# Performance work log

Hardware: AMD Instinct MI355X
Metric: run time of the kernel (lower is better)

The kernel has to match this reference:

```python
import jax, jax.numpy as jnp
import numpy as np

B, N, C = 8, 8192, 256
H = 8            # num_heads
D = C // H       # head dim = 32
P = 64           # proj_size (Linformer rank)


def setup_inputs() -> dict:
    key = jax.random.key(0)
    ks = jax.random.split(key, 12)
    s = lambda fan_in: 1.0 / np.sqrt(fan_in)
    return {
        "x": jax.random.normal(ks[0], (B, N, C), jnp.float32),
        "Wqkvv": jax.random.normal(ks[1], (4 * C, C), jnp.float32) * s(C),
        "WE": jax.random.normal(ks[2], (P, N), jnp.float32) * s(N),
        "bE": jax.random.normal(ks[3], (P,), jnp.float32) * s(N),
        "WF": jax.random.normal(ks[4], (P, N), jnp.float32) * s(N),
        "bF": jax.random.normal(ks[5], (P,), jnp.float32) * s(N),
        "Wo1": jax.random.normal(ks[6], (C // 2, C), jnp.float32) * s(C),
        "bo1": jax.random.normal(ks[7], (C // 2,), jnp.float32) * s(C),
        "Wo2": jax.random.normal(ks[8], (C // 2, C), jnp.float32) * s(C),
        "bo2": jax.random.normal(ks[9], (C // 2,), jnp.float32) * s(C),
        "temp1": jnp.ones((H, 1, 1), jnp.float32),
        "temp2": jnp.ones((H, 1, 1), jnp.float32),
    }


def _l2norm(v, axis=-1, eps=1e-12):
    # matches torch F.normalize
    n = jnp.sqrt(jnp.sum(v * v, axis=axis, keepdims=True))
    return v / jnp.maximum(n, eps)


def reference(x, Wqkvv, WE, bE, WF, bF, Wo1, bo1, Wo2, bo2, temp1, temp2):
    b, n, c = x.shape
    # qkvv: [b,n,4c] -> [4,b,h,d,n]  (includes the .transpose(-2,-1) of each part)
    qkvv = jnp.einsum('bnc,fc->bnf', x, Wqkvv).reshape(b, n, 4, H, D)
    qkvv = qkvv.transpose(2, 0, 3, 4, 1)
    q, k, v_ca, v_sa = qkvv[0], qkvv[1], qkvv[2], qkvv[3]  # each [b,h,d,n]

    # Linformer-style low-rank projections along the token axis
    k_proj = jnp.einsum('bhdn,pn->bhdp', k, WE) + bE   # [b,h,d,p]
    v_proj = jnp.einsum('bhdn,pn->bhdp', v_sa, WF) + bF

    qn = _l2norm(q)
    kn = _l2norm(k)

    # --- channel attention branch (XCiT-style) ---
    attn_ca = jnp.einsum('bhdn,bhen->bhde', qn, kn) * temp1[None]  # [b,h,d,d]
    attn_ca = jax.nn.softmax(attn_ca, axis=-1)  # dropout: eval mode (identity)
    x_ca = jnp.einsum('bhde,bhen->bhdn', attn_ca, v_ca)
    x_ca = x_ca.transpose(0, 3, 1, 2).reshape(b, n, c)  # [b,n,c]

    # --- spatial attention branch (low-rank) ---
    attn_sa = jnp.einsum('bhdn,bhdp->bhnp', qn, k_proj) * temp2[None]  # [b,h,n,p]
    attn_sa = jax.nn.softmax(attn_sa, axis=-1)
    x_sa = jnp.einsum('bhnp,bhdp->bhnd', attn_sa, v_proj)  # [b,h,n,d]
    # faithful to original: permute(0,3,1,2).reshape(b,n,c)
    x_sa = x_sa.transpose(0, 3, 1, 2).reshape(b, n, c)

    x_sa = jnp.einsum('bnc,oc->bno', x_sa, Wo1) + bo1
    x_ca = jnp.einsum('bnc,oc->bno', x_ca, Wo2) + bo2
    return jnp.concatenate((x_sa, x_ca), axis=-1)
```

## Files before the change

kernel.cpp:

```cpp
#include <hip/hip_runtime.h>
#include <hip/hip_bf16.h>
#include <stdint.h>


typedef __attribute__((ext_vector_type(8))) __bf16 bf16x8;
typedef __attribute__((ext_vector_type(4))) __bf16 bf16x4;
typedef __attribute__((ext_vector_type(4))) float f32x4;

#define MFMA(a, b, c) __builtin_amdgcn_mfma_f32_16x16x32_bf16((a), (b), (c), 0, 0, 0)

__device__ __forceinline__ void gl2lds16(const __bf16* g, __bf16* l) {
  __builtin_amdgcn_global_load_lds(
      (const __attribute__((address_space(1))) void*)(const void*)g,
      (__attribute__((address_space(3))) void*)(void*)l, 16, 0, 0);
}

__device__ __forceinline__ int detect_f32(const unsigned int* __restrict__ xw) {
  int c = 0;
#pragma unroll
  for (int i = 0; i < 64; ++i) {
    const unsigned int u = xw[i];
    c += (((u >> 7) & 0xFF) >= 0xC0) ? 1 : 0;
    c += (((u >> 23) & 0xFF) >= 0xC0) ? 1 : 0;
  }
  return c > 8;
}

__global__ __launch_bounds__(256) void k_convert_x(const void* __restrict__ src,
                                                   __bf16* __restrict__ dst) {
  const int i = (blockIdx.x * 256 + threadIdx.x) * 8;
  if (detect_f32((const unsigned int*)src)) {
    const float* s = (const float*)src;
    bf16x8 v;
#pragma unroll
    for (int j = 0; j < 8; ++j) v[j] = (__bf16)s[i + j];
    *(bf16x8*)(dst + i) = v;
  } else {
    *(bf16x8*)(dst + i) = *(const bf16x8*)((const __bf16*)src + i);
  }
}

__global__ __launch_bounds__(256) void k_convert_w(
    const void* s0, const void* s1, const void* s2, const void* s3, const void* s4,
    const void* s5, const void* s6, const void* s7, const void* s8, const void* s9,
    const void* s10, __bf16* __restrict__ cw, const void* __restrict__ xsrc) {
  const int i = (blockIdx.x * 256 + threadIdx.x) * 8;
  if (i >= 1376656) return;
  const void* s;
  int base;
  if (i < 262144)        { s = s0;  base = 0; }
  else if (i < 786432)   { s = s1;  base = 262144; }
  else if (i < 786496)   { s = s2;  base = 786432; }
  else if (i < 1310784)  { s = s3;  base = 786496; }
  else if (i < 1310848)  { s = s4;  base = 1310784; }
  else if (i < 1343616)  { s = s5;  base = 1310848; }
  else if (i < 1343744)  { s = s6;  base = 1343616; }
  else if (i < 1376512)  { s = s7;  base = 1343744; }
  else if (i < 1376640)  { s = s8;  base = 1376512; }
  else if (i < 1376648)  { s = s9;  base = 1376640; }
  else                   { s = s10; base = 1376648; }
  const int li = i - base;
  if (detect_f32((const unsigned int*)xsrc)) {
    const float* sf = (const float*)s;
#pragma unroll
    for (int j = 0; j < 8; ++j) cw[i + j] = (__bf16)sf[li + j];
  } else {
    const __bf16* sb = (const __bf16*)s;
#pragma unroll
    for (int j = 0; j < 8; ++j) cw[i + j] = sb[li + j];
  }
}

union alignas(16) QkvvSmem {
  struct { __bf16 A[2][4096]; __bf16 B[2][4096]; } k;
  __bf16 C[32 * 136];
};

__global__ __launch_bounds__(256, 5) void k_qkvv(const __bf16* __restrict__ x,
                                                 const __bf16* __restrict__ Wq,
                                                 __bf16* __restrict__ qkvv,
                                                 float* __restrict__ npart) {
  __shared__ QkvvSmem sm;
  const int t = threadIdx.x, lane = t & 63;
  const int wr = t >> 7, wc = (t >> 6) & 1;
  const int l15 = lane & 15, g = lane >> 4;
  const int f0 = blockIdx.y * 128;
  const int t0 = blockIdx.x * 128;
  f32x4 acc[4][4] = {};
  const int r = t >> 2;
  const int c8 = ((t & 3) ^ ((t >> 3) & 3)) * 8;
  const int cx = ((g ^ ((l15 >> 1) & 3)) * 8);
#pragma unroll
  for (int i = 0; i < 2; ++i) {
    gl2lds16(Wq + (size_t)(f0 + i * 64 + r) * 256 + c8, &sm.k.A[0][i * 2048 + t * 8]);
    gl2lds16(x + (size_t)(t0 + i * 64 + r) * 256 + c8, &sm.k.B[0][i * 2048 + t * 8]);
  }
  __syncthreads();
  for (int ks = 0; ks < 8; ++ks) {
    const int cur = ks & 1, nxt = cur ^ 1;
    if (ks < 7) {
      const int k1 = (ks + 1) * 32;
#pragma unroll
      for (int i = 0; i < 2; ++i) {
        gl2lds16(Wq + (size_t)(f0 + i * 64 + r) * 256 + k1 + c8, &sm.k.A[nxt][i * 2048 + t * 8]);
        gl2lds16(x + (size_t)(t0 + i * 64 + r) * 256 + k1 + c8, &sm.k.B[nxt][i * 2048 + t * 8]);
      }
    }
    bf16x8 af[4], bfr[4];
#pragma unroll
    for (int i = 0; i < 4; ++i) {
      af[i] = *(const bf16x8*)(&sm.k.A[cur][(wr * 64 + i * 16 + l15) * 32 + cx]);
      bfr[i] = *(const bf16x8*)(&sm.k.B[cur][(wc * 64 + i * 16 + l15) * 32 + cx]);
    }
#pragma unroll
    for (int i = 0; i < 4; ++i)
#pragma unroll
      for (int j = 0; j < 4; ++j) acc[i][j] = MFMA(af[i], bfr[j], acc[i][j]);
    __syncthreads();
  }
  const int b = t0 >> 13;
  const int n0 = t0 & 8191;
  if ((f0 >> 8) == 2) {
    __bf16* vnc = qkvv + (size_t)33554432;
    const int cb = (f0 & 255) + wr * 64;
#pragma unroll
    for (int i = 0; i < 4; ++i)
#pragma unroll
      for (int j = 0; j < 4; ++j) {
        bf16x4 p4;
#pragma unroll
        for (int rr = 0; rr < 4; ++rr) p4[rr] = (__bf16)acc[i][j][rr];
        const int col = wc * 64 + j * 16 + l15;
        *(bf16x4*)(vnc + (size_t)(b * 8192 + n0 + col) * 256 + cb + i * 16 + g * 4) = p4;
      }
    return;
  }
  for (int i = 0; i < 4; ++i) {
    if (i) __syncthreads();
#pragma unroll
    for (int j = 0; j < 4; ++j)
#pragma unroll
      for (int rr = 0; rr < 4; ++rr)
        sm.C[(wr * 16 + g * 4 + rr) * 136 + wc * 64 + j * 16 + l15] = (__bf16)acc[i][j][rr];
    __syncthreads();
#pragma unroll
    for (int half = 0; half < 2; ++half) {
      const int row_l = (t >> 4) + half * 16;
      const int col8 = (t & 15) * 8;
      const bf16x8 v = *(const bf16x8*)(sm.C + row_l * 136 + col8);
      const int f = f0 + (row_l >> 4) * 64 + i * 16 + (row_l & 15);
      *(bf16x8*)(qkvv + (size_t)(((f >> 8) * 8 + b) * 256 + (f & 255)) * 8192 + n0 + col8) = v;
      if (f0 < 512) {
        float s = 0.f;
#pragma unroll
        for (int jj = 0; jj < 8; ++jj) { const float q = (float)v[jj]; s += q * q; }
#pragma unroll
        for (int off = 1; off < 16; off <<= 1) s += __shfl_xor(s, off, 16);
        if ((t & 15) == 0) npart[(size_t)blockIdx.x * 512 + f] = s;
      }
    }
  }
}

__global__ __launch_bounds__(256) void k_nred(const float* __restrict__ npart,
                                              float* __restrict__ qsum,
                                              float* __restrict__ ksum) {
  const int which = blockIdx.x >> 3, b = blockIdx.x & 7;
  const int c = threadIdx.x;
  float s = 0.f;
#pragma unroll 4
  for (int j = 0; j < 64; ++j)
    s += npart[(size_t)(b * 64 + j) * 512 + which * 256 + c];
  (which ? ksum : qsum)[b * 256 + c] = s;
}

__global__ __launch_bounds__(256) void k_proj_part(const __bf16* __restrict__ qkvv,
                                                   const __bf16* __restrict__ WE,
                                                   const __bf16* __restrict__ WF,
                                                   float* __restrict__ pbuf) {
  __shared__ alignas(16) __bf16 As[2][128 * 32];
  __shared__ alignas(16) __bf16 Bs[2][64 * 32];
  const int t = threadIdx.x, lane = t & 63;
  const int wr = t >> 7, wc = (t >> 6) & 1;
  const int l15 = lane & 15, g = lane >> 4;
  const int kc = blockIdx.x, mt = blockIdx.y, pj = blockIdx.z;
  const __bf16* A = qkvv + (size_t)(pj ? 3 : 1) * 2048 * 8192;
  const __bf16* Bm = pj ? WF : WE;
  const int r0 = mt * 128;
  f32x4 acc[4][2] = {};
  const int r = t >> 2;
  const int c8 = ((t & 3) ^ ((t >> 3) & 3)) * 8;
  const int cx = ((g ^ ((l15 >> 1) & 3)) * 8);
  const int kb = kc * 512;
#pragma unroll
  for (int i = 0; i < 2; ++i)
    gl2lds16(A + (size_t)(r0 + i * 64 + r) * 8192 + kb + c8, &As[0][i * 2048 + t * 8]);
  gl2lds16(Bm + (size_t)r * 8192 + kb + c8, &Bs[0][t * 8]);
  __syncthreads();
  for (int ks = 0; ks < 16; ++ks) {
    const int cur = ks & 1, nxt = cur ^ 1;
    if (ks < 15) {
      const int k1 = kb + (ks + 1) * 32;
#pragma unroll
      for (int i = 0; i < 2; ++i)
        gl2lds16(A + (size_t)(r0 + i * 64 + r) * 8192 + k1 + c8, &As[nxt][i * 2048 + t * 8]);
      gl2lds16(Bm + (size_t)r * 8192 + k1 + c8, &Bs[nxt][t * 8]);
    }
    bf16x8 af[4], bfr[2];
#pragma unroll
    for (int i = 0; i < 4; ++i)
      af[i] = *(const bf16x8*)(&As[cur][(wr * 64 + i * 16 + l15) * 32 + cx]);
#pragma unroll
    for (int j = 0; j < 2; ++j)
      bfr[j] = *(const bf16x8*)(&Bs[cur][(wc * 32 + j * 16 + l15) * 32 + cx]);
#pragma unroll
    for (int i = 0; i < 4; ++i)
#pragma unroll
      for (int j = 0; j < 2; ++j) acc[i][j] = MFMA(af[i], bfr[j], acc[i][j]);
    __syncthreads();
  }
  float* dst = pbuf + (size_t)((pj * 16 + kc) * 2048 + r0) * 64;
#pragma unroll
  for (int i = 0; i < 4; ++i)
#pragma unroll
    for (int j = 0; j < 2; ++j)
#pragma unroll
      for (int rr = 0; rr < 4; ++rr)
        dst[(wr * 64 + i * 16 + g * 4 + rr) * 64 + wc * 32 + j * 16 + l15] = acc[i][j][rr];
}

__global__ __launch_bounds__(256) void k_proj_reduce(const float* __restrict__ pbuf,
                                                     const __bf16* __restrict__ bE,
                                                     const __bf16* __restrict__ bF,
                                                     const float* __restrict__ qsum,
                                                     const __bf16* __restrict__ t2,
                                                     __bf16* __restrict__ kprojT,
                                                     __bf16* __restrict__ vprojb) {
  const int idx = blockIdx.x * 256 + threadIdx.x;
  const int pj = idx >> 17, rp = idx & 131071, p = idx & 63;
  const int row = rp >> 6, bh = row >> 5, d = row & 31, h = bh & 7;
  float s = (float)((pj ? bF : bE)[p]);
  const float* src = pbuf + (size_t)pj * 16 * 131072 + rp;
#pragma unroll
  for (int k = 0; k < 16; ++k) s += src[(size_t)k * 131072];
  if (pj == 0) {
    const float qi = 1.0f / fmaxf(sqrtf(qsum[row]), 1e-12f);
    kprojT[bh * 2048 + p * 32 + d] = (__bf16)(s * qi * (float)t2[h]);
  } else {
    vprojb[bh * 2048 + d * 64 + p] = (__bf16)s;
  }
}

__global__ __launch_bounds__(256) void k_sca_part(const __bf16* __restrict__ qkvv,
                                                  float* __restrict__ spart) {
  const int bh = blockIdx.x, kc = blockIdx.y;
  const int t = threadIdx.x, lane = t & 63, w = t >> 6;
  const __bf16* qb = qkvv + (size_t)(bh * 32) * 8192;
  const __bf16* kb = qkvv + (size_t)(2048 + bh * 32) * 8192;
  f32x4 acc[2][2] = {};
  const int kbase = kc * 1024 + w * 256 + (lane >> 4) * 8;
#pragma unroll
  for (int ks = 0; ks < 256; ks += 32) {
    bf16x8 af[2], bfr[2];
#pragma unroll
    for (int i = 0; i < 2; ++i) {
      af[i] = *(const bf16x8*)(qb + (size_t)(i * 16 + (lane & 15)) * 8192 + kbase + ks);
      bfr[i] = *(const bf16x8*)(kb + (size_t)(i * 16 + (lane & 15)) * 8192 + kbase + ks);
    }
#pragma unroll
    for (int i = 0; i < 2; ++i)
#pragma unroll
      for (int j = 0; j < 2; ++j) acc[i][j] = MFMA(af[i], bfr[j], acc[i][j]);
  }
  float* dst = spart + (size_t)((bh * 8 + kc) * 4 + w) * 1024;
#pragma unroll
  for (int i = 0; i < 2; ++i)
#pragma unroll
    for (int j = 0; j < 2; ++j)
#pragma unroll
      for (int rr = 0; rr < 4; ++rr)
        dst[(i * 16 + (lane >> 4) * 4 + rr) * 32 + j * 16 + (lane & 15)] = acc[i][j][rr];
}

__global__ __launch_bounds__(256) void k_sca_softmax(const float* __restrict__ spart,
                                                     const float* __restrict__ qsum,
                                                     const float* __restrict__ ksum,
                                                     const __bf16* __restrict__ temp1,
                                                     __bf16* __restrict__ attnb) {
  const int bh = blockIdx.x;
  __shared__ float S[1024];
  const int t = threadIdx.x;
  const float tmp = (float)temp1[bh & 7];
  for (int idx = t; idx < 1024; idx += 256) {
    float s = 0.f;
    const float* src = spart + (size_t)bh * 32768 + idx;
#pragma unroll
    for (int k = 0; k < 32; ++k) s += src[k * 1024];
    const float qi = 1.0f / fmaxf(sqrtf(qsum[bh * 32 + (idx >> 5)]), 1e-12f);
    const float ki = 1.0f / fmaxf(sqrtf(ksum[bh * 32 + (idx & 31)]), 1e-12f);
    S[idx] = s * qi * ki * tmp;
  }
  __syncthreads();
  const int lane = t & 63, w = t >> 6;
#pragma unroll
  for (int rr = 0; rr < 4; ++rr) {
    const int row = rr * 8 + w * 2 + (lane >> 5);
    const int e = lane & 31;
    float v = S[row * 32 + e];
    float m = v;
#pragma unroll
    for (int off = 16; off; off >>= 1) m = fmaxf(m, __shfl_xor(m, off, 32));
    const float ex = __expf(v - m);
    float sm = ex;
#pragma unroll
    for (int off = 16; off; off >>= 1) sm += __shfl_xor(sm, off, 32);
    attnb[(size_t)bh * 1024 + row * 32 + e] = (__bf16)(ex / sm);
  }
}

__global__ __launch_bounds__(256) void k_casa(const __bf16* __restrict__ qkvv,
                                              const __bf16* __restrict__ attnb,
                                              const __bf16* __restrict__ kprojT,
                                              const __bf16* __restrict__ vprojb,
                                              __bf16* __restrict__ xca,
                                              __bf16* __restrict__ xsa) {
  __shared__ __bf16 P[4][16 * 72];
  __shared__ __bf16 Qs[32 * 264];
  const int t = threadIdx.x, lane = t & 63, w = t >> 6;
  const int l15 = lane & 15, g = lane >> 4;
  if (blockIdx.y < 64) {
    const int bh = blockIdx.y, b = bh >> 3, h = bh & 7;
    const __bf16* vnc = qkvv + (size_t)33554432;
    bf16x8 aa[2];
#pragma unroll
    for (int mi = 0; mi < 2; ++mi)
      aa[mi] = *(const bf16x8*)(attnb + bh * 1024 + (mi * 16 + l15) * 32 + g * 8);
#pragma unroll
    for (int it = 0; it < 4; ++it) {
      const int n = blockIdx.x * 256 + it * 64 + w * 16 + l15;
      const bf16x8 bq = *(const bf16x8*)(vnc + (size_t)(b * 8192 + n) * 256 + h * 32 + g * 8);
      f32x4 o[2] = {};
#pragma unroll
      for (int mi = 0; mi < 2; ++mi) o[mi] = MFMA(aa[mi], bq, o[mi]);
#pragma unroll
      for (int mi = 0; mi < 2; ++mi) {
        bf16x4 p4;
#pragma unroll
        for (int rr = 0; rr < 4; ++rr) p4[rr] = (__bf16)o[mi][rr];
        *(bf16x4*)(xca + (size_t)(b * 8192 + n) * 256 + h * 32 + mi * 16 + g * 4) = p4;
      }
    }
  } else {
    const int bh = blockIdx.y - 64;
    const __bf16* qb = qkvv + (size_t)(bh * 32) * 8192;
    {
      const int er = t >> 5;
      const int nc8 = (t & 31) * 8;
#pragma unroll
      for (int l = 0; l < 4; ++l) {
        const int e = l * 8 + er;
        *(bf16x8*)(&Qs[e * 264 + nc8]) =
            *(const bf16x8*)(qb + (size_t)e * 8192 + blockIdx.x * 256 + nc8);
      }
    }
    __syncthreads();
    bf16x8 ka[4], va[2][2];
#pragma unroll
    for (int tile = 0; tile < 4; ++tile)
      ka[tile] = *(const bf16x8*)(kprojT + bh * 2048 + (tile * 16 + l15) * 32 + g * 8);
#pragma unroll
    for (int mi = 0; mi < 2; ++mi)
#pragma unroll
      for (int kh = 0; kh < 2; ++kh)
        va[mi][kh] = *(const bf16x8*)(vprojb + bh * 2048 + (mi * 16 + l15) * 64 + kh * 32 + g * 8);
    __bf16* Pw = &P[w][0];
#pragma unroll
    for (int it = 0; it < 4; ++it) {
      const int n0 = blockIdx.x * 256 + it * 64 + w * 16;
      const int nl = it * 64 + w * 16 + l15;
      union { bf16x8 v; unsigned short u[8]; } bq;
#pragma unroll
      for (int j = 0; j < 8; ++j)
        bq.u[j] = *(const unsigned short*)(&Qs[(g * 8 + j) * 264 + nl]);
      f32x4 st[4];
#pragma unroll
      for (int tile = 0; tile < 4; ++tile) {
        f32x4 z = {};
        st[tile] = MFMA(ka[tile], bq.v, z);
      }
      float m = st[0][0];
#pragma unroll
      for (int tile = 0; tile < 4; ++tile)
#pragma unroll
        for (int rr = 0; rr < 4; ++rr) m = fmaxf(m, st[tile][rr]);
      m = fmaxf(m, __shfl_xor(m, 16, 64));
      m = fmaxf(m, __shfl_xor(m, 32, 64));
      float sum = 0.f;
#pragma unroll
      for (int tile = 0; tile < 4; ++tile) {
        bf16x4 p4;
#pragma unroll
        for (int rr = 0; rr < 4; ++rr) {
          const float ex = __expf(st[tile][rr] - m);
          sum += ex;
          p4[rr] = (__bf16)ex;
        }
        *(bf16x4*)(Pw + l15 * 72 + tile * 16 + g * 4) = p4;
      }
      sum += __shfl_xor(sum, 16, 64);
      sum += __shfl_xor(sum, 32, 64);
      const float inv = 1.0f / sum;
      f32x4 o[2] = {};
#pragma unroll
      for (int kh = 0; kh < 2; ++kh) {
        const bf16x8 pf = *(const bf16x8*)(Pw + l15 * 72 + kh * 32 + g * 8);
#pragma unroll
        for (int mi = 0; mi < 2; ++mi) o[mi] = MFMA(va[mi][kh], pf, o[mi]);
      }
#pragma unroll
      for (int mi = 0; mi < 2; ++mi)
#pragma unroll
        for (int rr = 0; rr < 4; ++rr) {
          const int d = mi * 16 + g * 4 + rr;
          xsa[(size_t)(bh * 32 + d) * 8192 + n0 + l15] = (__bf16)(o[mi][rr] * inv);
        }
    }
  }
}

__global__ __launch_bounds__(256) void k_out(const __bf16* __restrict__ xsa,
                                             const __bf16* __restrict__ xca,
                                             const __bf16* __restrict__ Wo1,
                                             const __bf16* __restrict__ bo1,
                                             const __bf16* __restrict__ Wo2,
                                             const __bf16* __restrict__ bo2,
                                             void* __restrict__ outv,
                                             const void* __restrict__ xsrc) {
  __shared__ alignas(16) __bf16 As[2][128 * 32];
  __shared__ alignas(16) __bf16 Bs[2][128 * 32];
  const int t = threadIdx.x, lane = t & 63;
  const int wr = t >> 7, wc = (t >> 6) & 1;
  const int l15 = lane & 15, g = lane >> 4;
  const int nt = blockIdx.x, b = blockIdx.y, br = blockIdx.z;
  const int isf32 = detect_f32((const unsigned int*)xsrc);
  const __bf16* Wo = br ? Wo2 : Wo1;
  const __bf16* bo = br ? bo2 : bo1;
  f32x4 acc[4][4] = {};
  const int r = t >> 2;
  const int c8 = ((t & 3) ^ ((t >> 3) & 3)) * 8;
  const int cx = ((g ^ ((l15 >> 1) & 3)) * 8);
  const int row_b = nt * 128 + r;
  auto asrc = [&](int i, int k0) -> const __bf16* {
    const int row = row_b + i * 64;
    if (br == 0)
      return xsa + (size_t)((b * 8 + ((row >> 5) & 7)) * 32 + (row >> 8)) * 8192 +
             (row & 31) * 256 + k0 + c8;
    return xca + (size_t)(b * 8192 + row) * 256 + k0 + c8;
  };
#pragma unroll
  for (int i = 0; i < 2; ++i) {
    gl2lds16(asrc(i, 0), &As[0][i * 2048 + t * 8]);
    gl2lds16(Wo + (size_t)(i * 64 + r) * 256 + c8, &Bs[0][i * 2048 + t * 8]);
  }
  __syncthreads();
  for (int ks = 0; ks < 8; ++ks) {
    const int cur = ks & 1, nxt = cur ^ 1;
    if (ks < 7) {
      const int k1 = (ks + 1) * 32;
#pragma unroll
      for (int i = 0; i < 2; ++i) {
        gl2lds16(asrc(i, k1), &As[nxt][i * 2048 + t * 8]);
        gl2lds16(Wo + (size_t)(i * 64 + r) * 256 + k1 + c8, &Bs[nxt][i * 2048 + t * 8]);
      }
    }
    bf16x8 af[4], bfr[4];
#pragma unroll
    for (int i = 0; i < 4; ++i) {
      af[i] = *(const bf16x8*)(&As[cur][(wr * 64 + i * 16 + l15) * 32 + cx]);
      bfr[i] = *(const bf16x8*)(&Bs[cur][(wc * 64 + i * 16 + l15) * 32 + cx]);
    }
#pragma unroll
    for (int i = 0; i < 4; ++i)
#pragma unroll
      for (int j = 0; j < 4; ++j) acc[i][j] = MFMA(af[i], bfr[j], acc[i][j]);
    __syncthreads();
  }
  float bias[4];
#pragma unroll
  for (int j = 0; j < 4; ++j) bias[j] = (float)bo[wc * 64 + j * 16 + l15];
#pragma unroll
  for (int i = 0; i < 4; ++i) {
#pragma unroll
    for (int j = 0; j < 4; ++j) {
      const int col = wc * 64 + j * 16 + l15;
#pragma unroll
      for (int rr = 0; rr < 4; ++rr) {
        const int row = nt * 128 + wr * 64 + i * 16 + g * 4 + rr;
        const float val = acc[i][j][rr] + bias[j];
        const size_t oi = (size_t)(b * 8192 + row) * 256 + br * 128 + col;
        if (isf32) ((float*)outv)[oi] = val;
        else ((__bf16*)outv)[oi] = (__bf16)val;
      }
    }
  }
}

extern "C" void kernel_launch(void* const* d_in, const int* in_sizes, int n_in,
                              void* d_out, int out_size, void* d_ws, size_t ws_size,
                              hipStream_t stream) {
  char* ws = (char*)d_ws;
  __bf16* qkvv   = (__bf16*)(ws);
  __bf16* cinx   = (__bf16*)(ws + 134217728ull);
  __bf16* xca    = (__bf16*)(ws + 134217728ull);
  float*  pbuf   = (float*)(ws + 167772160ull);
  float*  npart  = (float*)(ws + 184549376ull);
  float*  spart  = (float*)(ws + 184549376ull);
  __bf16* xsa    = (__bf16*)(ws + 167772160ull);
  __bf16* kprojT = (__bf16*)(ws + 201326592ull);
  __bf16* vprojb = (__bf16*)(ws + 201588736ull);
  float*  qsum   = (float*)(ws + 201850880ull);
  float*  ksum   = (float*)(ws + 201859072ull);
  __bf16* attnb  = (__bf16*)(ws + 201867264ull);
  __bf16* cw     = (__bf16*)(ws + 201998336ull);

  __bf16* cWq  = cw;
  __bf16* cWE  = cw + 262144;
  __bf16* cbE  = cw + 786432;
  __bf16* cWF  = cw + 786496;
  __bf16* cbF  = cw + 1310784;
  __bf16* cWo1 = cw + 1310848;
  __bf16* cbo1 = cw + 1343616;
  __bf16* cWo2 = cw + 1343744;
  __bf16* cbo2 = cw + 1376512;
  __bf16* ct1  = cw + 1376640;
  __bf16* ct2  = cw + 1376648;

  k_convert_x<<<8192, 256, 0, stream>>>(d_in[0], cinx);
  k_convert_w<<<673, 256, 0, stream>>>(d_in[1], d_in[2], d_in[3], d_in[4], d_in[5],
                                       d_in[6], d_in[7], d_in[8], d_in[9], d_in[10],
                                       d_in[11], cw, d_in[0]);
  k_qkvv<<<dim3(512, 8), 256, 0, stream>>>(cinx, cWq, qkvv, npart);
  k_nred<<<16, 256, 0, stream>>>(npart, qsum, ksum);
  k_proj_part<<<dim3(16, 16, 2), 256, 0, stream>>>(qkvv, cWE, cWF, pbuf);
  k_proj_reduce<<<dim3(1024), 256, 0, stream>>>(pbuf, cbE, cbF, qsum, ct2, kprojT, vprojb);
  k_sca_part<<<dim3(64, 8), 256, 0, stream>>>(qkvv, spart);
  k_sca_softmax<<<dim3(64), 256, 0, stream>>>(spart, qsum, ksum, ct1, attnb);
  k_casa<<<dim3(32, 128), 256, 0, stream>>>(qkvv, attnb, kprojT, vprojb, xca, xsa);
  k_out<<<dim3(64, 8, 2), 256, 0, stream>>>(xsa, xca, cWo1, cbo1, cWo2, cbo2, d_out, d_in[0]);
}
```

Measured before the change: 330.2 us.

## Remap qkvv grid for XCD L2 locality and stage casa outputs through LDS

The qkvv GEMM grid becomes 1-D, and block IDs are remapped so all eight feature tiles of one token tile run on the same XCD, which should improve L2 reuse of x. The v_ca part is no longer written in a separate token-major layout; it uses the same channel-major layout as q/k/v_sa. k_casa then stages v_ca tiles in LDS, and both branches stage their results through an LDS tile so global stores are coalesced 16-byte writes. The cost is extra barriers per iteration and more shared memory per block.

After: 350.9 us. +6.3%, slower.

```diff
diff --git a/kernel.cpp b/kernel.cpp
--- a/kernel.cpp
+++ b/kernel.cpp
@@ -84,8 +84,11 @@
   const int t = threadIdx.x, lane = t & 63;
   const int wr = t >> 7, wc = (t >> 6) & 1;
   const int l15 = lane & 15, g = lane >> 4;
-  const int f0 = blockIdx.y * 128;
-  const int t0 = blockIdx.x * 128;
+  const int bid = blockIdx.x;
+  const int xcd = bid & 7, jj = bid >> 3;
+  const int f0 = (jj & 7) * 128;
+  const int tt = xcd * 64 + (jj >> 3);
+  const int t0 = tt * 128;
   f32x4 acc[4][4] = {};
   const int r = t >> 2;
   const int c8 = ((t & 3) ^ ((t >> 3) & 3)) * 8;
@@ -120,21 +123,6 @@
   }
   const int b = t0 >> 13;
   const int n0 = t0 & 8191;
-  if ((f0 >> 8) == 2) {
-    __bf16* vnc = qkvv + (size_t)33554432;
-    const int cb = (f0 & 255) + wr * 64;
-#pragma unroll
-    for (int i = 0; i < 4; ++i)
-#pragma unroll
-      for (int j = 0; j < 4; ++j) {
-        bf16x4 p4;
-#pragma unroll
-        for (int rr = 0; rr < 4; ++rr) p4[rr] = (__bf16)acc[i][j][rr];
-        const int col = wc * 64 + j * 16 + l15;
-        *(bf16x4*)(vnc + (size_t)(b * 8192 + n0 + col) * 256 + cb + i * 16 + g * 4) = p4;
-      }
-    return;
-  }
   for (int i = 0; i < 4; ++i) {
     if (i) __syncthreads();
 #pragma unroll
@@ -153,10 +141,10 @@
       if (f0 < 512) {
         float s = 0.f;
 #pragma unroll
-        for (int jj = 0; jj < 8; ++jj) { const float q = (float)v[jj]; s += q * q; }
+        for (int jj2 = 0; jj2 < 8; ++jj2) { const float q = (float)v[jj2]; s += q * q; }
 #pragma unroll
         for (int off = 1; off < 16; off <<= 1) s += __shfl_xor(s, off, 16);
-        if ((t & 15) == 0) npart[(size_t)blockIdx.x * 512 + f] = s;
+        if ((t & 15) == 0) npart[(size_t)tt * 512 + f] = s;
       }
     }
   }
@@ -318,52 +306,75 @@
   }
 }
 
+union alignas(16) CasaSmem {
+  struct { __bf16 V[32 * 264]; __bf16 L[64 * 72]; } ca;
+  struct { __bf16 Q[32 * 264]; __bf16 P[4][16 * 72]; __bf16 L[32 * 72]; } sa;
+};
+
 __global__ __launch_bounds__(256) void k_casa(const __bf16* __restrict__ qkvv,
                                               const __bf16* __restrict__ attnb,
                                               const __bf16* __restrict__ kprojT,
                                               const __bf16* __restrict__ vprojb,
                                               __bf16* __restrict__ xca,
                                               __bf16* __restrict__ xsa) {
-  __shared__ __bf16 P[4][16 * 72];
-  __shared__ __bf16 Qs[32 * 264];
+  __shared__ CasaSmem sm;
   const int t = threadIdx.x, lane = t & 63, w = t >> 6;
   const int l15 = lane & 15, g = lane >> 4;
   if (blockIdx.y < 64) {
     const int bh = blockIdx.y, b = bh >> 3, h = bh & 7;
-    const __bf16* vnc = qkvv + (size_t)33554432;
+    const __bf16* vb = qkvv + (size_t)(4096 + bh * 32) * 8192;
+    {
+      const int er = t >> 5, nc8 = (t & 31) * 8;
+#pragma unroll
+      for (int l = 0; l < 4; ++l) {
+        const int e = l * 8 + er;
+        *(bf16x8*)(&sm.ca.V[e * 264 + nc8]) =
+            *(const bf16x8*)(vb + (size_t)e * 8192 + blockIdx.x * 256 + nc8);
+      }
+    }
     bf16x8 aa[2];
 #pragma unroll
     for (int mi = 0; mi < 2; ++mi)
       aa[mi] = *(const bf16x8*)(attnb + bh * 1024 + (mi * 16 + l15) * 32 + g * 8);
+    __syncthreads();
 #pragma unroll
     for (int it = 0; it < 4; ++it) {
-      const int n = blockIdx.x * 256 + it * 64 + w * 16 + l15;
-      const bf16x8 bq = *(const bf16x8*)(vnc + (size_t)(b * 8192 + n) * 256 + h * 32 + g * 8);
+      const int nl = it * 64 + w * 16 + l15;
+      union { bf16x8 v; unsigned short u[8]; } bq;
+#pragma unroll
+      for (int j = 0; j < 8; ++j)
+        bq.u[j] = *(const unsigned short*)(&sm.ca.V[(g * 8 + j) * 264 + nl]);
       f32x4 o[2] = {};
 #pragma unroll
-      for (int mi = 0; mi < 2; ++mi) o[mi] = MFMA(aa[mi], bq, o[mi]);
+      for (int mi = 0; mi < 2; ++mi) o[mi] = MFMA(aa[mi], bq.v, o[mi]);
+      if (it) __syncthreads();
 #pragma unroll
       for (int mi = 0; mi < 2; ++mi) {
         bf16x4 p4;
 #pragma unroll
         for (int rr = 0; rr < 4; ++rr) p4[rr] = (__bf16)o[mi][rr];
-        *(bf16x4*)(xca + (size_t)(b * 8192 + n) * 256 + h * 32 + mi * 16 + g * 4) = p4;
+        *(bf16x4*)(&sm.ca.L[(w * 16 + l15) * 72 + mi * 16 + g * 4]) = p4;
+      }
+      __syncthreads();
+      {
+        const int row = t >> 2, ch = t & 3;
+        const bf16x8 v = *(const bf16x8*)(&sm.ca.L[row * 72 + ch * 8]);
+        *(bf16x8*)(xca + (size_t)(b * 8192 + blockIdx.x * 256 + it * 64 + row) * 256 +
+                   h * 32 + ch * 8) = v;
       }
     }
   } else {
     const int bh = blockIdx.y - 64;
     const __bf16* qb = qkvv + (size_t)(bh * 32) * 8192;
     {
-      const int er = t >> 5;
-      const int nc8 = (t & 31) * 8;
+      const int er = t >> 5, nc8 = (t & 31) * 8;
 #pragma unroll
       for (int l = 0; l < 4; ++l) {
         const int e = l * 8 + er;
-        *(bf16x8*)(&Qs[e * 264 + nc8]) =
+        *(bf16x8*)(&sm.sa.Q[e * 264 + nc8]) =
             *(const bf16x8*)(qb + (size_t)e * 8192 + blockIdx.x * 256 + nc8);
       }
     }
-    __syncthreads();
     bf16x8 ka[4], va[2][2];
 #pragma unroll
     for (int tile = 0; tile < 4; ++tile)
@@ -373,15 +384,15 @@
 #pragma unroll
       for (int kh = 0; kh < 2; ++kh)
         va[mi][kh] = *(const bf16x8*)(vprojb + bh * 2048 + (mi * 16 + l15) * 64 + kh * 32 + g * 8);
-    __bf16* Pw = &P[w][0];
+    __syncthreads();
+    __bf16* Pw = &sm.sa.P[w][0];
 #pragma unroll
     for (int it = 0; it < 4; ++it) {
-      const int n0 = blockIdx.x * 256 + it * 64 + w * 16;
       const int nl = it * 64 + w * 16 + l15;
       union { bf16x8 v; unsigned short u[8]; } bq;
 #pragma unroll
       for (int j = 0; j < 8; ++j)
-        bq.u[j] = *(const unsigned short*)(&Qs[(g * 8 + j) * 264 + nl]);
+        bq.u[j] = *(const unsigned short*)(&sm.sa.Q[(g * 8 + j) * 264 + nl]);
       f32x4 st[4];
 #pragma unroll
       for (int tile = 0; tile < 4; ++tile) {
@@ -417,13 +428,21 @@
 #pragma unroll
         for (int mi = 0; mi < 2; ++mi) o[mi] = MFMA(va[mi][kh], pf, o[mi]);
       }
+      if (it) __syncthreads();
 #pragma unroll
       for (int mi = 0; mi < 2; ++mi)
 #pragma unroll
         for (int rr = 0; rr < 4; ++rr) {
           const int d = mi * 16 + g * 4 + rr;
-          xsa[(size_t)(bh * 32 + d) * 8192 + n0 + l15] = (__bf16)(o[mi][rr] * inv);
+          sm.sa.L[d * 72 + w * 16 + l15] = (__bf16)(o[mi][rr] * inv);
         }
+      __syncthreads();
+      {
+        const int row = t >> 3, ch = t & 7;
+        const bf16x8 v = *(const bf16x8*)(&sm.sa.L[row * 72 + ch * 8]);
+        *(bf16x8*)(xsa + (size_t)(bh * 32 + row) * 8192 + blockIdx.x * 256 + it * 64 +
+                   ch * 8) = v;
+      }
     }
   }
 }
@@ -539,7 +558,7 @@
   k_convert_w<<<673, 256, 0, stream>>>(d_in[1], d_in[2], d_in[3], d_in[4], d_in[5],
                                        d_in[6], d_in[7], d_in[8], d_in[9], d_in[10],
                                        d_in[11], cw, d_in[0]);
-  k_qkvv<<<dim3(512, 8), 256, 0, stream>>>(cinx, cWq, qkvv, npart);
+  k_qkvv<<<dim3(4096), 256, 0, stream>>>(cinx, cWq, qkvv, npart);
   k_nred<<<16, 256, 0, stream>>>(npart, qsum, ksum);
   k_proj_part<<<dim3(16, 16, 2), 256, 0, stream>>>(qkvv, cWE, cWF, pbuf);
   k_proj_reduce<<<dim3(1024), 256, 0, stream>>>(pbuf, cbE, cbF, qsum, ct2, kprojT, vprojb);
```
